# Kernel tuning notes

Measured on AMD Instinct MI355X. Metric: run time of the kernel, lower is better.

The kernel has to match this reference:

```python
import jax, jax.numpy as jnp
import numpy as np

N_NODES = 1_000_000   # nodal points, 3 DOFs each
N_ELEMS = 500_000     # H8 (8-node hexahedral) elements
N_TYPES = 64          # distinct element stiffness matrices (24x24)


def setup_inputs() -> dict:
    key = jax.random.key(0)
    k1, k2, k3, k4 = jax.random.split(key, 4)
    U = jax.random.normal(k1, (N_NODES, 3), dtype=jnp.float32)
    filters = jax.random.normal(k2, (N_TYPES, 24, 24), dtype=jnp.float32)
    H8types = jax.random.randint(k3, (N_ELEMS,), 0, N_TYPES, dtype=jnp.int32)
    nodIdx = jax.random.randint(k4, (N_ELEMS, 8), 0, N_NODES, dtype=jnp.int32)
    return {"U": U, "filters": filters, "H8types": H8types, "nodIdx": nodIdx}


def reference(U, filters, H8types, nodIdx):
    """FEM stiffness matvec KU = sum_e scatter(K_type(e) @ gather(U, e)).

    U:       [N, 3]      nodal displacements (3 DOFs per node)
    filters: [T, 24, 24] per-type element stiffness matrices
    H8types: [E]         element type index into filters
    nodIdx:  [E, 8]      element -> node connectivity
    returns KU: [N, 3]
    """
    E = nodIdx.shape[0]
    # gather the 8 nodes x 3 DOFs of each element -> [E, 24]
    ue = U[nodIdx].reshape(E, 24)
    # per-type stiffness for each element -> [E, 24, 24]
    Ke = filters[H8types]
    # per-element force vector f_e = K_e @ u_e -> [E, 24]
    fe = jnp.einsum('eij,ej->ei', Ke, ue)
    # scatter-add element forces back to nodal DOFs
    KU = jnp.zeros_like(U).at[nodIdx.reshape(-1)].add(fe.reshape(E * 8, 3))
    return KU
```

## Files before the change

kernel.cpp:

```cpp
#include <hip/hip_runtime.h>


#define NTYPES    64
#define KSTRIDE   580
#define RSHIFT    10
#define RNODES    1024
#define MAXB      1024
#define CAP       5120
#define K1_TPB    1024
#define K1_EPT    2
#define K1_CHUNK  (K1_TPB * K1_EPT)
#define K2_TPB    512
#define PREP_TPB  256

typedef int          nint4  __attribute__((ext_vector_type(4)));
typedef unsigned int nuint2 __attribute__((ext_vector_type(2)));

__device__ __forceinline__ unsigned bf16_rne(float f) {
    unsigned b = __float_as_uint(f);
    return (b + 0x7FFFu + ((b >> 16) & 1u)) >> 16;
}


__global__ __launch_bounds__(PREP_TPB) void pack_u_kernel(
    const float* __restrict__ U, nuint2* __restrict__ Ub,
    float* __restrict__ KU, unsigned* __restrict__ tails,
    int n_nodes, int n_buckets)
{
    int n = blockIdx.x * PREP_TPB + threadIdx.x;
    if (n < n_buckets) tails[n] = 0;
    if (n >= n_nodes) return;
    const float* up = U + (size_t)n * 3;
    unsigned bx = bf16_rne(up[0]);
    unsigned by = bf16_rne(up[1]);
    unsigned bz = bf16_rne(up[2]);
    nuint2 v = { bx | (by << 16), bz };
    Ub[n] = v;
    KU[3 * n + 0] = 0.f;
    KU[3 * n + 1] = 0.f;
    KU[3 * n + 2] = 0.f;
}


__global__ __launch_bounds__(K1_TPB, 4) void feconv_bin_kernel(
    const nuint2* __restrict__ Ub,
    const float* __restrict__ K,
    const int*   __restrict__ types,
    const int*   __restrict__ nodIdx,
    float*       __restrict__ KU,
    unsigned*    __restrict__ tails,
    nuint2*      __restrict__ recs,
    int n_elems, int n_buckets)
{
    extern __shared__ float sK[];
    __shared__ unsigned sCnt[MAXB];
    __shared__ unsigned sBase[MAXB];

    for (int w = threadIdx.x; w < NTYPES * 576; w += K1_TPB) {
        int t = w / 576;
        int r = w - t * 576;
        sK[t * KSTRIDE + r] = K[w];
    }
    for (int i = threadIdx.x; i < n_buckets; i += K1_TPB) sCnt[i] = 0;
    __syncthreads();

    const int e0 = blockIdx.x * K1_CHUNK + threadIdx.x;
    int     nodes[K1_EPT][8];
    int     tt[K1_EPT];
    nuint2  uu[K1_EPT][8];

#pragma unroll
    for (int k = 0; k < K1_EPT; ++k) {
        int e = e0 + k * K1_TPB;
        tt[k] = -1;
        if (e < n_elems) {
            tt[k] = __builtin_nontemporal_load(&types[e]);
            const nint4* q = (const nint4*)(nodIdx + (size_t)e * 8);
            nint4 a = __builtin_nontemporal_load(q);
            nint4 b = __builtin_nontemporal_load(q + 1);
            nodes[k][0] = a.x; nodes[k][1] = a.y; nodes[k][2] = a.z; nodes[k][3] = a.w;
            nodes[k][4] = b.x; nodes[k][5] = b.y; nodes[k][6] = b.z; nodes[k][7] = b.w;
#pragma unroll
            for (int j = 0; j < 8; ++j)
                uu[k][j] = Ub[nodes[k][j]];
#pragma unroll
            for (int j = 0; j < 8; ++j)
                atomicAdd(&sCnt[(unsigned)nodes[k][j] >> RSHIFT], 1u);
        }
    }
    __syncthreads();

    for (int b = threadIdx.x; b < n_buckets; b += K1_TPB) {
        unsigned c = sCnt[b];
        sBase[b] = c ? atomicAdd(&tails[b], c) : 0u;
        sCnt[b] = 0;
    }
    __syncthreads();

#pragma unroll
    for (int k = 0; k < K1_EPT; ++k) {
        if (tt[k] < 0) continue;

        float ue[24];
#pragma unroll
        for (int j = 0; j < 8; ++j) {
            nuint2 v = uu[k][j];
            ue[3 * j + 0] = __uint_as_float(v.x << 16);
            ue[3 * j + 1] = __uint_as_float(v.x & 0xFFFF0000u);
            ue[3 * j + 2] = __uint_as_float(v.y << 16);
        }

        const float4* Kt4 = (const float4*)(sK + tt[k] * KSTRIDE);
#pragma unroll
        for (int j = 0; j < 8; ++j) {
            float a0 = 0.f, a1 = 0.f, a2 = 0.f;
#pragma unroll
            for (int q = 0; q < 6; ++q) {
                float4 k0 = Kt4[(3 * j + 0) * 6 + q];
                float4 k1 = Kt4[(3 * j + 1) * 6 + q];
                float4 k2 = Kt4[(3 * j + 2) * 6 + q];
                float u0 = ue[4 * q + 0], u1 = ue[4 * q + 1];
                float u2 = ue[4 * q + 2], u3 = ue[4 * q + 3];
                a0 += k0.x * u0 + k0.y * u1 + k0.z * u2 + k0.w * u3;
                a1 += k1.x * u0 + k1.y * u1 + k1.z * u2 + k1.w * u3;
                a2 += k2.x * u0 + k2.y * u1 + k2.z * u2 + k2.w * u3;
            }
            unsigned n = (unsigned)nodes[k][j];
            unsigned b = n >> RSHIFT;
            unsigned pos = sBase[b] + atomicAdd(&sCnt[b], 1u);
            if (pos < CAP) {
                unsigned local = n & (RNODES - 1);
                nuint2 r = { bf16_rne(a0) | (bf16_rne(a1) << 16),
                             bf16_rne(a2) | (local << 16) };
                recs[(size_t)b * CAP + pos] = r;
            } else {
                atomicAdd(&KU[(size_t)n * 3 + 0], a0);
                atomicAdd(&KU[(size_t)n * 3 + 1], a1);
                atomicAdd(&KU[(size_t)n * 3 + 2], a2);
            }
        }
    }
}


__global__ __launch_bounds__(K2_TPB) void feconv_acc_kernel(
    const nuint2*   __restrict__ recs,
    const unsigned* __restrict__ tails,
    float*          __restrict__ KU,
    int n_nodes)
{
    __shared__ float sAcc[RNODES * 3];
    const int b = blockIdx.x;

    for (int i = threadIdx.x; i < RNODES * 3; i += K2_TPB) sAcc[i] = 0.f;
    __syncthreads();

    unsigned cnt = tails[b];
    if (cnt > CAP) cnt = CAP;
    const nuint2* base = recs + (size_t)b * CAP;
    for (unsigned i = threadIdx.x; i < cnt; i += K2_TPB) {
        nuint2 r = base[i];
        unsigned o = (r.y >> 16) * 3;
        atomicAdd(&sAcc[o + 0], __uint_as_float(r.x << 16));
        atomicAdd(&sAcc[o + 1], __uint_as_float(r.x & 0xFFFF0000u));
        atomicAdd(&sAcc[o + 2], __uint_as_float(r.y << 16));
    }
    __syncthreads();

    const int nbase = b * RNODES;
    int limit = n_nodes - nbase;
    if (limit > RNODES) limit = RNODES;
    limit *= 3;
    float* out = KU + (size_t)nbase * 3;
    for (int i = threadIdx.x; i < limit; i += K2_TPB) out[i] += sAcc[i];
}


__global__ __launch_bounds__(256) void feconv_elem_kernel(
    const float* __restrict__ U, const float* __restrict__ K,
    const int* __restrict__ types, const int* __restrict__ nodIdx,
    float* __restrict__ KU, int n_elems)
{
    int e = blockIdx.x * blockDim.x + threadIdx.x;
    if (e >= n_elems) return;
    int t = types[e];
    const int4* idx4 = (const int4*)(nodIdx + (size_t)e * 8);
    int4 iA = idx4[0], iB = idx4[1];
    int nodes[8] = {iA.x, iA.y, iA.z, iA.w, iB.x, iB.y, iB.z, iB.w};
    float ue[24];
#pragma unroll
    for (int j = 0; j < 8; ++j) {
        const float* up = U + (size_t)nodes[j] * 3;
        ue[3 * j + 0] = up[0]; ue[3 * j + 1] = up[1]; ue[3 * j + 2] = up[2];
    }
    const float* Kt = K + (size_t)t * 576;
#pragma unroll
    for (int i = 0; i < 24; ++i) {
        const float4* row = (const float4*)(Kt + i * 24);
        float acc = 0.f;
#pragma unroll
        for (int q = 0; q < 6; ++q) {
            float4 k = row[q];
            acc += k.x * ue[4 * q + 0] + k.y * ue[4 * q + 1]
                 + k.z * ue[4 * q + 2] + k.w * ue[4 * q + 3];
        }
        atomicAdd(&KU[(size_t)nodes[i / 3] * 3 + (i % 3)], acc);
    }
}

extern "C" void kernel_launch(void* const* d_in, const int* in_sizes, int n_in,
                              void* d_out, int out_size, void* d_ws, size_t ws_size,
                              hipStream_t stream) {
    const float* U      = (const float*)d_in[0];
    const float* Kf     = (const float*)d_in[1];
    const int*   types  = (const int*)d_in[2];
    const int*   nodIdx = (const int*)d_in[3];
    float*       KU     = (float*)d_out;

    const int n_elems = in_sizes[2];
    const int n_nodes = in_sizes[0] / 3;
    const int n_buckets = (n_nodes + RNODES - 1) / RNODES;

    const size_t ub_off  = 8192;
    const size_t rec_off = ub_off + (((size_t)n_nodes * 8 + 255) & ~255ull);
    const size_t need    = rec_off + (size_t)n_buckets * CAP * 8;

    if (n_buckets <= MAXB && ws_size >= need) {
        unsigned* tails = (unsigned*)d_ws;
        nuint2*   Ub    = (nuint2*)((char*)d_ws + ub_off);
        nuint2*   recs  = (nuint2*)((char*)d_ws + rec_off);

        int gridP = (n_nodes + PREP_TPB - 1) / PREP_TPB;
        pack_u_kernel<<<gridP, PREP_TPB, 0, stream>>>(
            U, Ub, KU, tails, n_nodes, n_buckets);

        size_t lds_bytes = (size_t)NTYPES * KSTRIDE * sizeof(float);
        int grid1 = (n_elems + K1_CHUNK - 1) / K1_CHUNK;
        feconv_bin_kernel<<<grid1, K1_TPB, lds_bytes, stream>>>(
            Ub, Kf, types, nodIdx, KU, tails, recs, n_elems, n_buckets);
        feconv_acc_kernel<<<n_buckets, K2_TPB, 0, stream>>>(
            recs, tails, KU, n_nodes);
    } else {
        (void)hipMemsetAsync(KU, 0, (size_t)out_size * sizeof(float), stream);
        int block = 256;
        int grid = (n_elems + block - 1) / block;
        feconv_elem_kernel<<<grid, block, 0, stream>>>(
            U, Kf, types, nodIdx, KU, n_elems);
    }
}
```

Baseline: 218.6 us.

## Fuse pack, bin, and accumulate into one cooperative persistent kernel

Replaces the three launches (pack U to bf16, bin element forces into node buckets, per-bucket shared-memory accumulate) with a single cooperative kernel that uses grid-wide syncs between phases and a persistent grid of at most 256 blocks looping over chunks and buckets. Bucket size is doubled to 2048 nodes with matching capacity, so there are half as many buckets. The aim is to remove launch gaps and per-launch reloading of the stiffness matrices into LDS, since each persistent block loads them only once. In exchange, occupancy drops to one 1024-thread block per CU, grid syncs add cost, and each chunk iteration pays extra block barriers and per-bucket global atomics. Cooperative launch can also fail if the grid does not fit co-resident.

```diff
diff --git a/kernel.cpp b/kernel.cpp
--- a/kernel.cpp
+++ b/kernel.cpp
@@ -1,17 +1,18 @@
 #include <hip/hip_runtime.h>
+#include <hip/hip_cooperative_groups.h>
+
+namespace cg = cooperative_groups;
 
 
 #define NTYPES    64
 #define KSTRIDE   580
-#define RSHIFT    10
-#define RNODES    1024
-#define MAXB      1024
-#define CAP       5120
-#define K1_TPB    1024
-#define K1_EPT    2
-#define K1_CHUNK  (K1_TPB * K1_EPT)
-#define K2_TPB    512
-#define PREP_TPB  256
+#define RSHIFT    11
+#define RNODES    2048
+#define MAXB      512
+#define CAP       10240
+#define TPB       1024
+#define EPT       2
+#define CHUNK     (TPB * EPT)
 
 typedef int          nint4  __attribute__((ext_vector_type(4)));
 typedef unsigned int nuint2 __attribute__((ext_vector_type(2)));
@@ -21,158 +22,156 @@
     return (b + 0x7FFFu + ((b >> 16) & 1u)) >> 16;
 }
 
-
-__global__ __launch_bounds__(PREP_TPB) void pack_u_kernel(
-    const float* __restrict__ U, nuint2* __restrict__ Ub,
-    float* __restrict__ KU, unsigned* __restrict__ tails,
-    int n_nodes, int n_buckets)
-{
-    int n = blockIdx.x * PREP_TPB + threadIdx.x;
-    if (n < n_buckets) tails[n] = 0;
-    if (n >= n_nodes) return;
-    const float* up = U + (size_t)n * 3;
-    unsigned bx = bf16_rne(up[0]);
-    unsigned by = bf16_rne(up[1]);
-    unsigned bz = bf16_rne(up[2]);
-    nuint2 v = { bx | (by << 16), bz };
-    Ub[n] = v;
-    KU[3 * n + 0] = 0.f;
-    KU[3 * n + 1] = 0.f;
-    KU[3 * n + 2] = 0.f;
-}
-
-
-__global__ __launch_bounds__(K1_TPB, 4) void feconv_bin_kernel(
-    const nuint2* __restrict__ Ub,
+__global__ __launch_bounds__(TPB, 1) void feconv_fused_kernel(
+    const float* __restrict__ U,
     const float* __restrict__ K,
     const int*   __restrict__ types,
     const int*   __restrict__ nodIdx,
     float*       __restrict__ KU,
     unsigned*    __restrict__ tails,
+    nuint2*      __restrict__ Ub,
     nuint2*      __restrict__ recs,
-    int n_elems, int n_buckets)
+    int n_elems, int n_nodes, int n_buckets, int n_chunks)
 {
     extern __shared__ float sK[];
     __shared__ unsigned sCnt[MAXB];
     __shared__ unsigned sBase[MAXB];
 
-    for (int w = threadIdx.x; w < NTYPES * 576; w += K1_TPB) {
+    cg::grid_group grid = cg::this_grid();
+    const int tid      = threadIdx.x;
+    const int nthreads = gridDim.x * TPB;
+    const int gtid     = blockIdx.x * TPB + tid;
+
+    for (int n = gtid; n < n_nodes; n += nthreads) {
+        const float* up = U + (size_t)n * 3;
+        unsigned bx = bf16_rne(up[0]);
+        unsigned by = bf16_rne(up[1]);
+        unsigned bz = bf16_rne(up[2]);
+        nuint2 v = { bx | (by << 16), bz };
+        Ub[n] = v;
+        KU[3 * n + 0] = 0.f;
+        KU[3 * n + 1] = 0.f;
+        KU[3 * n + 2] = 0.f;
+    }
+    for (int b = gtid; b < n_buckets; b += nthreads) tails[b] = 0;
+    for (int w = tid; w < NTYPES * 576; w += TPB) {
         int t = w / 576;
         int r = w - t * 576;
         sK[t * KSTRIDE + r] = K[w];
     }
-    for (int i = threadIdx.x; i < n_buckets; i += K1_TPB) sCnt[i] = 0;
-    __syncthreads();
-
-    const int e0 = blockIdx.x * K1_CHUNK + threadIdx.x;
-    int     nodes[K1_EPT][8];
-    int     tt[K1_EPT];
-    nuint2  uu[K1_EPT][8];
-
-#pragma unroll
-    for (int k = 0; k < K1_EPT; ++k) {
-        int e = e0 + k * K1_TPB;
-        tt[k] = -1;
-        if (e < n_elems) {
-            tt[k] = __builtin_nontemporal_load(&types[e]);
-            const nint4* q = (const nint4*)(nodIdx + (size_t)e * 8);
-            nint4 a = __builtin_nontemporal_load(q);
-            nint4 b = __builtin_nontemporal_load(q + 1);
-            nodes[k][0] = a.x; nodes[k][1] = a.y; nodes[k][2] = a.z; nodes[k][3] = a.w;
-            nodes[k][4] = b.x; nodes[k][5] = b.y; nodes[k][6] = b.z; nodes[k][7] = b.w;
-#pragma unroll
-            for (int j = 0; j < 8; ++j)
-                uu[k][j] = Ub[nodes[k][j]];
-#pragma unroll
-            for (int j = 0; j < 8; ++j)
-                atomicAdd(&sCnt[(unsigned)nodes[k][j] >> RSHIFT], 1u);
-        }
-    }
-    __syncthreads();
-
-    for (int b = threadIdx.x; b < n_buckets; b += K1_TPB) {
-        unsigned c = sCnt[b];
-        sBase[b] = c ? atomicAdd(&tails[b], c) : 0u;
-        sCnt[b] = 0;
-    }
-    __syncthreads();
-
-#pragma unroll
-    for (int k = 0; k < K1_EPT; ++k) {
-        if (tt[k] < 0) continue;
-
-        float ue[24];
-#pragma unroll
-        for (int j = 0; j < 8; ++j) {
-            nuint2 v = uu[k][j];
-            ue[3 * j + 0] = __uint_as_float(v.x << 16);
-            ue[3 * j + 1] = __uint_as_float(v.x & 0xFFFF0000u);
-            ue[3 * j + 2] = __uint_as_float(v.y << 16);
-        }
-
-        const float4* Kt4 = (const float4*)(sK + tt[k] * KSTRIDE);
-#pragma unroll
-        for (int j = 0; j < 8; ++j) {
-            float a0 = 0.f, a1 = 0.f, a2 = 0.f;
-#pragma unroll
-            for (int q = 0; q < 6; ++q) {
-                float4 k0 = Kt4[(3 * j + 0) * 6 + q];
-                float4 k1 = Kt4[(3 * j + 1) * 6 + q];
-                float4 k2 = Kt4[(3 * j + 2) * 6 + q];
-                float u0 = ue[4 * q + 0], u1 = ue[4 * q + 1];
-                float u2 = ue[4 * q + 2], u3 = ue[4 * q + 3];
-                a0 += k0.x * u0 + k0.y * u1 + k0.z * u2 + k0.w * u3;
-                a1 += k1.x * u0 + k1.y * u1 + k1.z * u2 + k1.w * u3;
-                a2 += k2.x * u0 + k2.y * u1 + k2.z * u2 + k2.w * u3;
+
+    grid.sync();
+
+    for (int c = blockIdx.x; c < n_chunks; c += gridDim.x) {
+        __syncthreads();
+        for (int i = tid; i < n_buckets; i += TPB) sCnt[i] = 0;
+        __syncthreads();
+
+        const int e0 = c * CHUNK + tid;
+        int     nodes[EPT][8];
+        int     tt[EPT];
+        nuint2  uu[EPT][8];
+
+#pragma unroll
+        for (int k = 0; k < EPT; ++k) {
+            int e = e0 + k * TPB;
+            tt[k] = -1;
+            if (e < n_elems) {
+                tt[k] = __builtin_nontemporal_load(&types[e]);
+                const nint4* q = (const nint4*)(nodIdx + (size_t)e * 8);
+                nint4 a = __builtin_nontemporal_load(q);
+                nint4 b = __builtin_nontemporal_load(q + 1);
+                nodes[k][0] = a.x; nodes[k][1] = a.y; nodes[k][2] = a.z; nodes[k][3] = a.w;
+                nodes[k][4] = b.x; nodes[k][5] = b.y; nodes[k][6] = b.z; nodes[k][7] = b.w;
+#pragma unroll
+                for (int j = 0; j < 8; ++j)
+                    uu[k][j] = Ub[nodes[k][j]];
+#pragma unroll
+                for (int j = 0; j < 8; ++j)
+                    atomicAdd(&sCnt[(unsigned)nodes[k][j] >> RSHIFT], 1u);
             }
-            unsigned n = (unsigned)nodes[k][j];
-            unsigned b = n >> RSHIFT;
-            unsigned pos = sBase[b] + atomicAdd(&sCnt[b], 1u);
-            if (pos < CAP) {
-                unsigned local = n & (RNODES - 1);
-                nuint2 r = { bf16_rne(a0) | (bf16_rne(a1) << 16),
-                             bf16_rne(a2) | (local << 16) };
-                recs[(size_t)b * CAP + pos] = r;
-            } else {
-                atomicAdd(&KU[(size_t)n * 3 + 0], a0);
-                atomicAdd(&KU[(size_t)n * 3 + 1], a1);
-                atomicAdd(&KU[(size_t)n * 3 + 2], a2);
+        }
+        __syncthreads();
+
+        for (int b = tid; b < n_buckets; b += TPB) {
+            unsigned cc = sCnt[b];
+            sBase[b] = cc ? atomicAdd(&tails[b], cc) : 0u;
+            sCnt[b] = 0;
+        }
+        __syncthreads();
+
+#pragma unroll
+        for (int k = 0; k < EPT; ++k) {
+            if (tt[k] < 0) continue;
+
+            float ue[24];
+#pragma unroll
+            for (int j = 0; j < 8; ++j) {
+                nuint2 v = uu[k][j];
+                ue[3 * j + 0] = __uint_as_float(v.x << 16);
+                ue[3 * j + 1] = __uint_as_float(v.x & 0xFFFF0000u);
+                ue[3 * j + 2] = __uint_as_float(v.y << 16);
             }
-        }
-    }
-}
-
-
-__global__ __launch_bounds__(K2_TPB) void feconv_acc_kernel(
-    const nuint2*   __restrict__ recs,
-    const unsigned* __restrict__ tails,
-    float*          __restrict__ KU,
-    int n_nodes)
-{
-    __shared__ float sAcc[RNODES * 3];
-    const int b = blockIdx.x;
-
-    for (int i = threadIdx.x; i < RNODES * 3; i += K2_TPB) sAcc[i] = 0.f;
-    __syncthreads();
-
-    unsigned cnt = tails[b];
-    if (cnt > CAP) cnt = CAP;
-    const nuint2* base = recs + (size_t)b * CAP;
-    for (unsigned i = threadIdx.x; i < cnt; i += K2_TPB) {
-        nuint2 r = base[i];
-        unsigned o = (r.y >> 16) * 3;
-        atomicAdd(&sAcc[o + 0], __uint_as_float(r.x << 16));
-        atomicAdd(&sAcc[o + 1], __uint_as_float(r.x & 0xFFFF0000u));
-        atomicAdd(&sAcc[o + 2], __uint_as_float(r.y << 16));
-    }
-    __syncthreads();
-
-    const int nbase = b * RNODES;
-    int limit = n_nodes - nbase;
-    if (limit > RNODES) limit = RNODES;
-    limit *= 3;
-    float* out = KU + (size_t)nbase * 3;
-    for (int i = threadIdx.x; i < limit; i += K2_TPB) out[i] += sAcc[i];
+
+            const float4* Kt4 = (const float4*)(sK + tt[k] * KSTRIDE);
+#pragma unroll
+            for (int j = 0; j < 8; ++j) {
+                float a0 = 0.f, a1 = 0.f, a2 = 0.f;
+#pragma unroll
+                for (int q = 0; q < 6; ++q) {
+                    float4 k0 = Kt4[(3 * j + 0) * 6 + q];
+                    float4 k1 = Kt4[(3 * j + 1) * 6 + q];
+                    float4 k2 = Kt4[(3 * j + 2) * 6 + q];
+                    float u0 = ue[4 * q + 0], u1 = ue[4 * q + 1];
+                    float u2 = ue[4 * q + 2], u3 = ue[4 * q + 3];
+                    a0 += k0.x * u0 + k0.y * u1 + k0.z * u2 + k0.w * u3;
+                    a1 += k1.x * u0 + k1.y * u1 + k1.z * u2 + k1.w * u3;
+                    a2 += k2.x * u0 + k2.y * u1 + k2.z * u2 + k2.w * u3;
+                }
+                unsigned n = (unsigned)nodes[k][j];
+                unsigned b = n >> RSHIFT;
+                unsigned pos = sBase[b] + atomicAdd(&sCnt[b], 1u);
+                if (pos < CAP) {
+                    unsigned local = n & (RNODES - 1);
+                    nuint2 r = { bf16_rne(a0) | (bf16_rne(a1) << 16),
+                                 bf16_rne(a2) | (local << 16) };
+                    recs[(size_t)b * CAP + pos] = r;
+                } else {
+                    atomicAdd(&KU[(size_t)n * 3 + 0], a0);
+                    atomicAdd(&KU[(size_t)n * 3 + 1], a1);
+                    atomicAdd(&KU[(size_t)n * 3 + 2], a2);
+                }
+            }
+        }
+    }
+
+    grid.sync();
+
+    float* sAcc = sK;
+    for (int b = blockIdx.x; b < n_buckets; b += gridDim.x) {
+        __syncthreads();
+        for (int i = tid; i < RNODES * 3; i += TPB) sAcc[i] = 0.f;
+        __syncthreads();
+
+        unsigned cnt = tails[b];
+        if (cnt > CAP) cnt = CAP;
+        const nuint2* base = recs + (size_t)b * CAP;
+        for (unsigned i = tid; i < cnt; i += TPB) {
+            nuint2 r = base[i];
+            unsigned o = (r.y >> 16) * 3;
+            atomicAdd(&sAcc[o + 0], __uint_as_float(r.x << 16));
+            atomicAdd(&sAcc[o + 1], __uint_as_float(r.x & 0xFFFF0000u));
+            atomicAdd(&sAcc[o + 2], __uint_as_float(r.y << 16));
+        }
+        __syncthreads();
+
+        const int nbase = b * RNODES;
+        int limit = n_nodes - nbase;
+        if (limit > RNODES) limit = RNODES;
+        limit *= 3;
+        float* out = KU + (size_t)nbase * 3;
+        for (int i = tid; i < limit; i += TPB) out[i] += sAcc[i];
+    }
 }
 
 
@@ -217,11 +216,12 @@
     const int*   nodIdx = (const int*)d_in[3];
     float*       KU     = (float*)d_out;
 
-    const int n_elems = in_sizes[2];
-    const int n_nodes = in_sizes[0] / 3;
-    const int n_buckets = (n_nodes + RNODES - 1) / RNODES;
-
-    const size_t ub_off  = 8192;
+    int n_elems  = in_sizes[2];
+    int n_nodes  = in_sizes[0] / 3;
+    int n_buckets = (n_nodes + RNODES - 1) / RNODES;
+    int n_chunks  = (n_elems + CHUNK - 1) / CHUNK;
+
+    const size_t ub_off  = 4096;
     const size_t rec_off = ub_off + (((size_t)n_nodes * 8 + 255) & ~255ull);
     const size_t need    = rec_off + (size_t)n_buckets * CAP * 8;
 
@@ -230,16 +230,16 @@
         nuint2*   Ub    = (nuint2*)((char*)d_ws + ub_off);
         nuint2*   recs  = (nuint2*)((char*)d_ws + rec_off);
 
-        int gridP = (n_nodes + PREP_TPB - 1) / PREP_TPB;
-        pack_u_kernel<<<gridP, PREP_TPB, 0, stream>>>(
-            U, Ub, KU, tails, n_nodes, n_buckets);
-
         size_t lds_bytes = (size_t)NTYPES * KSTRIDE * sizeof(float);
-        int grid1 = (n_elems + K1_CHUNK - 1) / K1_CHUNK;
-        feconv_bin_kernel<<<grid1, K1_TPB, lds_bytes, stream>>>(
-            Ub, Kf, types, nodIdx, KU, tails, recs, n_elems, n_buckets);
-        feconv_acc_kernel<<<n_buckets, K2_TPB, 0, stream>>>(
-            recs, tails, KU, n_nodes);
+        int grid = n_chunks < 256 ? n_chunks : 256;
+
+        void* args[] = { (void*)&U, (void*)&Kf, (void*)&types, (void*)&nodIdx,
+                         (void*)&KU, (void*)&tails, (void*)&Ub, (void*)&recs,
+                         (void*)&n_elems, (void*)&n_nodes, (void*)&n_buckets,
+                         (void*)&n_chunks };
+        (void)hipLaunchCooperativeKernel((void*)feconv_fused_kernel,
+                                         dim3(grid), dim3(TPB),
+                                         args, (unsigned)lds_bytes, stream);
     } else {
         (void)hipMemsetAsync(KU, 0, (size_t)out_size * sizeof(float), stream);
         int block = 256;
```

Measured after the change: 299.9 us. +37.2%, slower.
